# Optimization experiments

Measured on AMD Instinct MI355X. Metric: run time of the kernel, lower is better.

The kernel has to match this reference:

```python
import jax, jax.numpy as jnp
import numpy as np

B, NPER, F, D, E, NUM_STEPS = 256, 512, 256, 32, 524288, 4
N = B * NPER
INIT_TAU, TAU_SCALE, STEP_ALPHA = 0.1, 0.5, 5.0


def setup_inputs() -> dict:
    key = jax.random.key(0)
    ks = jax.random.split(key, 10)
    x_start = jax.random.uniform(ks[0], (N,), jnp.float32, 0.1, 1.0)   # strictly positive iterate
    x_solution = jax.random.uniform(ks[1], (N,), jnp.float32, 0.0, 1.0)
    q = jax.random.normal(ks[2], (N,), jnp.float32)
    edge_src = jax.random.randint(ks[3], (E,), 0, N, jnp.int32)
    edge_dst = jax.random.randint(ks[4], (E,), 0, N, jnp.int32)
    vals_batch = jnp.repeat(jnp.arange(B, dtype=jnp.int32), NPER)      # equal-sized graphs
    proj_matrix = jax.random.normal(ks[5], (B, NPER, F), jnp.float32) / np.float32(np.sqrt(NPER))
    W_in = jax.random.normal(ks[6], (2, D), jnp.float32) / np.float32(np.sqrt(2.0))
    b_in = jnp.zeros((D,), jnp.float32)
    W_msg = jax.random.normal(ks[7], (D, D), jnp.float32) / np.float32(np.sqrt(D))
    b_msg = jnp.zeros((D,), jnp.float32)
    W_out = jax.random.normal(ks[8], (D, 1), jnp.float32) / np.float32(np.sqrt(D))
    b_out = jnp.zeros((1,), jnp.float32)
    return {"x_start": x_start, "x_solution": x_solution, "q": q,
            "proj_matrix": proj_matrix, "W_in": W_in, "b_in": b_in,
            "W_msg": W_msg, "b_msg": b_msg, "W_out": W_out, "b_out": b_out,
            "edge_src": edge_src, "edge_dst": edge_dst, "vals_batch": vals_batch}


def _l1_normalize(x, batch):
    # per-graph L1 normalization: x / sum_i |x_i| over the graph segment
    s = jax.ops.segment_sum(jnp.abs(x), batch, num_segments=B)
    return x / (s[batch] + 1e-12)


def _line_search(x, d, batch, max_alpha):
    # largest per-graph alpha s.t. x + alpha*d >= 0, capped at max_alpha
    ratio = jnp.where(d < 0, x / jnp.maximum(-d, 1e-12), max_alpha)
    a = jnp.clip(jax.ops.segment_min(ratio, batch, num_segments=B), 0.0, max_alpha)
    return a[batch]  # gathered back to per-node


def _gnn(xs, q, edge_src, edge_dst, W_in, b_in, W_msg, b_msg, W_out, b_out):
    h = jax.nn.relu(jnp.stack([xs, q], axis=-1) @ W_in + b_in)      # [N, D]
    m = h[edge_src] @ W_msg + b_msg                                  # [E, D]
    agg = jax.ops.segment_sum(m, edge_dst, num_segments=N)          # [N, D]
    h2 = jax.nn.relu(h + agg)
    return h2 @ W_out[:, 0] + b_out[0]                               # [N]


def reference(x_start, x_solution, q, proj_matrix, W_in, b_in, W_msg, b_msg,
              W_out, b_out, edge_src, edge_dst, vals_batch):
    tau = INIT_TAU
    xs = x_start
    preds, labels = [], []
    for _ in range(NUM_STEPS):
        pred = _gnn(xs, q, edge_src, edge_dst, W_in, b_in, W_msg, b_msg, W_out, b_out)
        preds.append(pred)
        labels.append(_l1_normalize(x_solution - xs, vals_batch))
        p = _l1_normalize(jax.lax.stop_gradient(pred), vals_batch)   # .detach() in torch
        direction = p + 3.0 * tau / (xs + tau)
        tau = max(tau * TAU_SCALE, 1e-5)
        # to_dense_batch with equal graph sizes == reshape; project onto nullspace basis
        dd = direction.reshape(B, NPER)
        df = jnp.einsum('bnf,bn->bf', proj_matrix, dd)               # [B, F]
        pproj = jnp.einsum('bnf,bf->bn', proj_matrix, df).reshape(-1)  # [N]
        alpha = _line_search(xs, pproj, vals_batch, STEP_ALPHA) * 0.995
        xs = xs + alpha * pproj
    return jnp.stack(preds, axis=1), jnp.stack(labels, axis=1)       # each [N, NUM_STEPS]
```

## Files before the change

kernel.cpp:

```cpp
#include <hip/hip_runtime.h>

#define BB 256
#define NPER 512
#define FF 256
#define DD 32
#define EE 524288
#define NN (BB*NPER)
#define NSTEPS 4

__device__ __forceinline__ float bflo(unsigned u) { return __uint_as_float(u << 16); }
__device__ __forceinline__ float bfhi(unsigned u) { return __uint_as_float(u & 0xFFFF0000u); }
__device__ __forceinline__ unsigned rtn_bf16(unsigned u) {
    return (u + 0x7FFFu + ((u >> 16) & 1u)) >> 16;
}


__global__ void k_degpack(const int* __restrict__ dst, unsigned* __restrict__ deg,
                          const float* __restrict__ xs0, const float* __restrict__ q,
                          float2* __restrict__ xq) {
    int t = blockIdx.x * blockDim.x + threadIdx.x;
    if (t < NN) { float2 v; v.x = xs0[t]; v.y = q[t]; xq[t] = v; }
    atomicAdd(&deg[dst[t]], 1u);
}

__global__ __launch_bounds__(256) void k_alloc(const unsigned* __restrict__ deg,
                                               unsigned* __restrict__ gcur,
                                               unsigned* __restrict__ rowstart,
                                               unsigned* __restrict__ cursor) {
    __shared__ unsigned r[256];
    __shared__ unsigned base;
    int t = threadIdx.x;
    int i = blockIdx.x * 256 + t;
    unsigned d = deg[i];
    r[t] = d;
    __syncthreads();
    for (int o = 1; o < 256; o <<= 1) {
        unsigned v = (t >= o) ? r[t - o] : 0u;
        __syncthreads();
        r[t] += v;
        __syncthreads();
    }
    if (t == 255) base = atomicAdd(gcur, r[255]);
    __syncthreads();
    unsigned excl = r[t] - d + base;
    rowstart[i] = excl;
    cursor[i] = excl;
}

__global__ void k_fill(const int* __restrict__ src, const int* __restrict__ dst,
                       unsigned* __restrict__ cursor, int* __restrict__ csr_src) {
    int e = blockIdx.x * blockDim.x + threadIdx.x;
    unsigned pos = atomicAdd(&cursor[dst[e]], 1u);
    csr_src[pos] = src[e];
}

template<int MODE>
__global__ __launch_bounds__(1024) void k_mega(const float* __restrict__ Pf,
                                               unsigned short* __restrict__ Pbf,
                                               const float2* __restrict__ xq_cur,
                                               float2* __restrict__ xq_nxt,
                                               const float* __restrict__ xsol,
                                               const float* __restrict__ Win,
                                               const float* __restrict__ bin,
                                               const float* __restrict__ Wmsg,
                                               const float* __restrict__ bmsg,
                                               const float* __restrict__ Wout,
                                               const float* __restrict__ bout,
                                               const unsigned* __restrict__ rowstart,
                                               const unsigned* __restrict__ deg,
                                               const int* __restrict__ csr_src,
                                               float* __restrict__ out_preds,
                                               float* __restrict__ out_labels,
                                               float tau, int step) {
    __shared__ float pred_l[NPER];
    __shared__ float dd_l[NPER], x_l[NPER], pp_l[NPER];
    __shared__ float sl[16 * FF];
    __shared__ float dfl[FF];
    __shared__ float redA[16], redB[16];
    int b = blockIdx.x;
    int t = threadIdx.x;
    int w = t >> 6, lane = t & 63;
    int gbase = b * NPER;

    {
        int d = lane & 31;
        int half = lane >> 5;
        float w0 = Win[d], w1 = Win[DD + d], b0 = bin[d];
        float wcol[DD];
        #pragma unroll
        for (int k = 0; k < DD; ++k) wcol[k] = Wmsg[k * DD + d];
        float wo = Wout[d];
        for (int pass = 0; pass < 16; ++pass) {
            int node = pass * 32 + w * 2 + half;
            int i = gbase + node;
            unsigned rs = rowstart[i];
            unsigned dg = deg[i];
            unsigned nfull = dg < 32u ? dg : 32u;
            float xv = 0.f, qv = 0.f;
            if ((unsigned)d < nfull) {
                int sv = csr_src[rs + d];
                float2 v = xq_cur[sv];
                xv = v.x; qv = v.y;
            }
            float s = 0.f;
            for (unsigned j = 0; j < nfull; ++j) {
                float xj = __shfl(xv, (int)j, 32);
                float qj = __shfl(qv, (int)j, 32);
                s += fmaxf(xj * w0 + qj * w1 + b0, 0.f);
            }
            for (unsigned j = 32; j < dg; ++j) {
                int sv = csr_src[rs + j];
                float2 v = xq_cur[sv];
                s += fmaxf(v.x * w0 + v.y * w1 + b0, 0.f);
            }
            float2 self = xq_cur[i];
            float hval = fmaxf(self.x * w0 + self.y * w1 + b0, 0.f);
            float agg = (float)dg * bmsg[d];
            #pragma unroll
            for (int k = 0; k < DD; ++k) agg += __shfl(s, k, 32) * wcol[k];
            float h2 = fmaxf(hval + agg, 0.f);
            float v = h2 * wo;
            #pragma unroll
            for (int o = 16; o > 0; o >>= 1) v += __shfl_down(v, o, 32);
            if (d == 0) {
                float pr = v + bout[0];
                pred_l[node] = pr;
                out_preds[(size_t)i * NSTEPS + step] = pr;
            }
        }
    }
    __syncthreads();

    float x = 0.f, r = 0.f, p = 0.f, a1 = 0.f, a2 = 0.f;
    if (t < NPER) {
        x = xq_cur[gbase + t].x;
        r = xsol[gbase + t] - x;
        p = pred_l[t];
        a1 = fabsf(r); a2 = fabsf(p);
    }
    #pragma unroll
    for (int o = 32; o > 0; o >>= 1) {
        a1 += __shfl_down(a1, o, 64);
        a2 += __shfl_down(a2, o, 64);
    }
    if (lane == 0) { redA[w] = a1; redB[w] = a2; }
    __syncthreads();
    float Sr = 1e-12f, Sp = 1e-12f;
    #pragma unroll
    for (int k = 0; k < 16; ++k) { Sr += redA[k]; Sp += redB[k]; }
    if (t < NPER) out_labels[(size_t)(gbase + t) * NSTEPS + step] = r / Sr;
    if (MODE == 2) return;
    if (t < NPER) {
        x_l[t] = x;
        dd_l[t] = p / Sp + 3.0f * tau / (x + tau);
    }
    __syncthreads();

    size_t pbase = ((size_t)(gbase + w * 32)) * FF + 4 * lane;
    float4 acc = {0.f, 0.f, 0.f, 0.f};
    if (MODE == 0) {
        const float4* Pr = (const float4*)(Pf + pbase);
        uint2* Pw = (uint2*)(Pbf + pbase);
        #pragma unroll
        for (int nb = 0; nb < 4; ++nb) {
            float4 pv[8];
            #pragma unroll
            for (int k = 0; k < 8; ++k) pv[k] = Pr[(size_t)(nb * 8 + k) * 64];
            #pragma unroll
            for (int k = 0; k < 8; ++k) {
                int n = nb * 8 + k;
                float sc = dd_l[w * 32 + n];
                acc.x += pv[k].x * sc; acc.y += pv[k].y * sc;
                acc.z += pv[k].z * sc; acc.w += pv[k].w * sc;
                unsigned u0 = rtn_bf16(__float_as_uint(pv[k].x));
                unsigned u1 = rtn_bf16(__float_as_uint(pv[k].y));
                unsigned u2 = rtn_bf16(__float_as_uint(pv[k].z));
                unsigned u3 = rtn_bf16(__float_as_uint(pv[k].w));
                uint2 o2; o2.x = u0 | (u1 << 16); o2.y = u2 | (u3 << 16);
                Pw[(size_t)n * 64] = o2;
            }
        }
    } else {
        const uint2* Pr = (const uint2*)(Pbf + pbase);
        #pragma unroll
        for (int nb = 0; nb < 4; ++nb) {
            uint2 pv[8];
            #pragma unroll
            for (int k = 0; k < 8; ++k) pv[k] = Pr[(size_t)(nb * 8 + k) * 64];
            #pragma unroll
            for (int k = 0; k < 8; ++k) {
                float sc = dd_l[w * 32 + nb * 8 + k];
                acc.x += bflo(pv[k].x) * sc; acc.y += bfhi(pv[k].x) * sc;
                acc.z += bflo(pv[k].y) * sc; acc.w += bfhi(pv[k].y) * sc;
            }
        }
    }
    ((float4*)sl)[w * 64 + lane] = acc;
    __syncthreads();
    if (t < FF) {
        float v = 0.f;
        #pragma unroll
        for (int k = 0; k < 16; ++k) v += sl[k * FF + t];
        dfl[t] = v;
    }
    __syncthreads();

    {
        int g = t >> 5, l5 = t & 31;
        int w2 = g >> 1, h = g & 1;
        float4 dfa = ((const float4*)dfl)[l5 * 2];
        float4 dfb4 = ((const float4*)dfl)[l5 * 2 + 1];
        const uint4* Pbase = (const uint4*)(Pbf + (size_t)(gbase + w2 * 32) * FF) + l5;
        #pragma unroll
        for (int nb = 0; nb < 4; ++nb) {
            uint4 pv[4];
            int off[4];
            #pragma unroll
            for (int k = 0; k < 4; ++k) {
                int idx = nb * 4 + k;
                off[k] = (idx < 8) ? (16 + 8 * h + idx) : (8 * h + idx - 8);
                pv[k] = Pbase[(size_t)off[k] * 32];
            }
            #pragma unroll
            for (int k = 0; k < 4; ++k) {
                float a = bflo(pv[k].x) * dfa.x + bfhi(pv[k].x) * dfa.y
                        + bflo(pv[k].y) * dfa.z + bfhi(pv[k].y) * dfa.w
                        + bflo(pv[k].z) * dfb4.x + bfhi(pv[k].z) * dfb4.y
                        + bflo(pv[k].w) * dfb4.z + bfhi(pv[k].w) * dfb4.w;
                #pragma unroll
                for (int o = 16; o > 0; o >>= 1) a += __shfl_down(a, o, 32);
                if (l5 == 0) pp_l[w2 * 32 + off[k]] = a;
            }
        }
    }
    __syncthreads();

    float d = 0.f, m = 5.0f;
    if (t < NPER) {
        d = pp_l[t];
        m = (d < 0.f) ? (x_l[t] / fmaxf(-d, 1e-12f)) : 5.0f;
    }
    #pragma unroll
    for (int o = 32; o > 0; o >>= 1) m = fminf(m, __shfl_down(m, o, 64));
    if (lane == 0) redA[w] = m;
    __syncthreads();
    float mm = redA[0];
    #pragma unroll
    for (int k = 1; k < 16; ++k) mm = fminf(mm, redA[k]);
    float alpha = fminf(fmaxf(mm, 0.f), 5.0f) * 0.995f;
    if (t < NPER) {
        float2 o2;
        o2.x = x_l[t] + alpha * d;
        o2.y = xq_cur[gbase + t].y;
        xq_nxt[gbase + t] = o2;
    }
}


extern "C" void kernel_launch(void* const* d_in, const int* in_sizes, int n_in,
                              void* d_out, int out_size, void* d_ws, size_t ws_size,
                              hipStream_t stream) {
    const float* x_start = (const float*)d_in[0];
    const float* x_sol   = (const float*)d_in[1];
    const float* q       = (const float*)d_in[2];
    const float* P       = (const float*)d_in[3];
    const float* Win     = (const float*)d_in[4];
    const float* bin     = (const float*)d_in[5];
    const float* Wmsg    = (const float*)d_in[6];
    const float* bmsg    = (const float*)d_in[7];
    const float* Wout    = (const float*)d_in[8];
    const float* bout    = (const float*)d_in[9];
    const int*   esrc    = (const int*)d_in[10];
    const int*   edst    = (const int*)d_in[11];

    float* out_preds  = (float*)d_out;
    float* out_labels = (float*)d_out + (size_t)NN * NSTEPS;

    float* w = (float*)d_ws;
    unsigned* deg  = (unsigned*)w; w += NN;
    unsigned* gcur = (unsigned*)w; w += 2;
    float2* xqA = (float2*)w; w += 2 * (size_t)NN;
    float2* xqB = (float2*)w; w += 2 * (size_t)NN;
    unsigned* rowstart = (unsigned*)w; w += NN;
    unsigned* cursor   = (unsigned*)w; w += NN;
    int* csr_src       = (int*)w;      w += EE;
    unsigned short* Pbf = (unsigned short*)w;

    hipMemsetAsync(deg, 0, (NN + 2) * sizeof(unsigned), stream);
    k_degpack<<<EE / 256, 256, 0, stream>>>(edst, deg, x_start, q, xqA);
    k_alloc<<<NN / 256, 256, 0, stream>>>(deg, gcur, rowstart, cursor);
    k_fill<<<EE / 256, 256, 0, stream>>>(esrc, edst, cursor, csr_src);

    k_mega<0><<<BB, 1024, 0, stream>>>(P, Pbf, xqA, xqB, x_sol, Win, bin, Wmsg, bmsg,
                                       Wout, bout, rowstart, deg, csr_src,
                                       out_preds, out_labels, 0.1f, 0);
    k_mega<1><<<BB, 1024, 0, stream>>>(P, Pbf, xqB, xqA, x_sol, Win, bin, Wmsg, bmsg,
                                       Wout, bout, rowstart, deg, csr_src,
                                       out_preds, out_labels, 0.05f, 1);
    k_mega<1><<<BB, 1024, 0, stream>>>(P, Pbf, xqA, xqB, x_sol, Win, bin, Wmsg, bmsg,
                                       Wout, bout, rowstart, deg, csr_src,
                                       out_preds, out_labels, 0.025f, 2);
    k_mega<2><<<BB, 1024, 0, stream>>>(P, Pbf, xqB, (float2*)nullptr, x_sol, Win, bin,
                                       Wmsg, bmsg, Wout, bout, rowstart, deg, csr_src,
                                       out_preds, out_labels, 0.0125f, 3);
}
```

Before: 491.2 us.

## Cache half of bf16 projection slab in LDS and move final-step labels earlier

The first projection pass now also writes the bf16 projection rows for the first 256 nodes of each graph into a 128 KB shared-memory slab. The second projection pass reads those rows from LDS instead of re-reading them from global memory; the other half still comes from global. The last-step labels are now computed at the end of the third kernel from the updated iterate, so the final kernel only runs the GNN and returns early. The large LDS allocation may limit occupancy to one 1024-thread block per CU and adds extra shared-memory writes in the first pass.

```diff
diff --git a/kernel.cpp b/kernel.cpp
--- a/kernel.cpp
+++ b/kernel.cpp
@@ -71,12 +71,13 @@
                                                const int* __restrict__ csr_src,
                                                float* __restrict__ out_preds,
                                                float* __restrict__ out_labels,
-                                               float tau, int step) {
+                                               float tau, int step, int last) {
     __shared__ float pred_l[NPER];
     __shared__ float dd_l[NPER], x_l[NPER], pp_l[NPER];
     __shared__ float sl[16 * FF];
     __shared__ float dfl[FF];
     __shared__ float redA[16], redB[16];
+    __shared__ unsigned short slabL[(MODE < 2 ? 256 : 1) * FF];
     int b = blockIdx.x;
     int t = threadIdx.x;
     int w = t >> 6, lane = t & 63;
@@ -129,6 +130,7 @@
             }
         }
     }
+    if (MODE == 2) return;
     __syncthreads();
 
     float x = 0.f, r = 0.f, p = 0.f, a1 = 0.f, a2 = 0.f;
@@ -148,15 +150,15 @@
     float Sr = 1e-12f, Sp = 1e-12f;
     #pragma unroll
     for (int k = 0; k < 16; ++k) { Sr += redA[k]; Sp += redB[k]; }
-    if (t < NPER) out_labels[(size_t)(gbase + t) * NSTEPS + step] = r / Sr;
-    if (MODE == 2) return;
     if (t < NPER) {
+        out_labels[(size_t)(gbase + t) * NSTEPS + step] = r / Sr;
         x_l[t] = x;
         dd_l[t] = p / Sp + 3.0f * tau / (x + tau);
     }
     __syncthreads();
 
     size_t pbase = ((size_t)(gbase + w * 32)) * FF + 4 * lane;
+    unsigned short* slw = slabL + (size_t)(w * 32) * FF + 4 * lane;
     float4 acc = {0.f, 0.f, 0.f, 0.f};
     if (MODE == 0) {
         const float4* Pr = (const float4*)(Pf + pbase);
@@ -178,6 +180,7 @@
                 unsigned u3 = rtn_bf16(__float_as_uint(pv[k].w));
                 uint2 o2; o2.x = u0 | (u1 << 16); o2.y = u2 | (u3 << 16);
                 Pw[(size_t)n * 64] = o2;
+                if (w < 8) *(uint2*)(slw + (size_t)n * FF) = o2;
             }
         }
     } else {
@@ -189,9 +192,11 @@
             for (int k = 0; k < 8; ++k) pv[k] = Pr[(size_t)(nb * 8 + k) * 64];
             #pragma unroll
             for (int k = 0; k < 8; ++k) {
-                float sc = dd_l[w * 32 + nb * 8 + k];
+                int n = nb * 8 + k;
+                float sc = dd_l[w * 32 + n];
                 acc.x += bflo(pv[k].x) * sc; acc.y += bfhi(pv[k].x) * sc;
                 acc.z += bflo(pv[k].y) * sc; acc.w += bfhi(pv[k].y) * sc;
+                if (w < 8) *(uint2*)(slw + (size_t)n * FF) = pv[k];
             }
         }
     }
@@ -210,26 +215,51 @@
         int w2 = g >> 1, h = g & 1;
         float4 dfa = ((const float4*)dfl)[l5 * 2];
         float4 dfb4 = ((const float4*)dfl)[l5 * 2 + 1];
-        const uint4* Pbase = (const uint4*)(Pbf + (size_t)(gbase + w2 * 32) * FF) + l5;
-        #pragma unroll
-        for (int nb = 0; nb < 4; ++nb) {
-            uint4 pv[4];
-            int off[4];
-            #pragma unroll
-            for (int k = 0; k < 4; ++k) {
-                int idx = nb * 4 + k;
-                off[k] = (idx < 8) ? (16 + 8 * h + idx) : (8 * h + idx - 8);
-                pv[k] = Pbase[(size_t)off[k] * 32];
-            }
-            #pragma unroll
-            for (int k = 0; k < 4; ++k) {
-                float a = bflo(pv[k].x) * dfa.x + bfhi(pv[k].x) * dfa.y
-                        + bflo(pv[k].y) * dfa.z + bfhi(pv[k].y) * dfa.w
-                        + bflo(pv[k].z) * dfb4.x + bfhi(pv[k].z) * dfb4.y
-                        + bflo(pv[k].w) * dfb4.z + bfhi(pv[k].w) * dfb4.w;
+        if (g < 16) {
+            const uint4* Lb = (const uint4*)(slabL + (size_t)(w2 * 32) * FF) + l5;
+            #pragma unroll
+            for (int nb = 0; nb < 4; ++nb) {
+                uint4 pv[4];
+                int off[4];
                 #pragma unroll
-                for (int o = 16; o > 0; o >>= 1) a += __shfl_down(a, o, 32);
-                if (l5 == 0) pp_l[w2 * 32 + off[k]] = a;
+                for (int k = 0; k < 4; ++k) {
+                    int idx = nb * 4 + k;
+                    off[k] = (idx < 8) ? (16 + 8 * h + idx) : (8 * h + idx - 8);
+                    pv[k] = Lb[(size_t)off[k] * 32];
+                }
+                #pragma unroll
+                for (int k = 0; k < 4; ++k) {
+                    float a = bflo(pv[k].x) * dfa.x + bfhi(pv[k].x) * dfa.y
+                            + bflo(pv[k].y) * dfa.z + bfhi(pv[k].y) * dfa.w
+                            + bflo(pv[k].z) * dfb4.x + bfhi(pv[k].z) * dfb4.y
+                            + bflo(pv[k].w) * dfb4.z + bfhi(pv[k].w) * dfb4.w;
+                    #pragma unroll
+                    for (int o = 16; o > 0; o >>= 1) a += __shfl_down(a, o, 32);
+                    if (l5 == 0) pp_l[w2 * 32 + off[k]] = a;
+                }
+            }
+        } else {
+            const uint4* Pbase = (const uint4*)(Pbf + (size_t)(gbase + w2 * 32) * FF) + l5;
+            #pragma unroll
+            for (int nb = 0; nb < 4; ++nb) {
+                uint4 pv[4];
+                int off[4];
+                #pragma unroll
+                for (int k = 0; k < 4; ++k) {
+                    int idx = nb * 4 + k;
+                    off[k] = (idx < 8) ? (16 + 8 * h + idx) : (8 * h + idx - 8);
+                    pv[k] = Pbase[(size_t)off[k] * 32];
+                }
+                #pragma unroll
+                for (int k = 0; k < 4; ++k) {
+                    float a = bflo(pv[k].x) * dfa.x + bfhi(pv[k].x) * dfa.y
+                            + bflo(pv[k].y) * dfa.z + bfhi(pv[k].y) * dfa.w
+                            + bflo(pv[k].z) * dfb4.x + bfhi(pv[k].z) * dfb4.y
+                            + bflo(pv[k].w) * dfb4.z + bfhi(pv[k].w) * dfb4.w;
+                    #pragma unroll
+                    for (int o = 16; o > 0; o >>= 1) a += __shfl_down(a, o, 32);
+                    if (l5 == 0) pp_l[w2 * 32 + off[k]] = a;
+                }
             }
         }
     }
@@ -248,11 +278,26 @@
     #pragma unroll
     for (int k = 1; k < 16; ++k) mm = fminf(mm, redA[k]);
     float alpha = fminf(fmaxf(mm, 0.f), 5.0f) * 0.995f;
+    float xnew = 0.f;
     if (t < NPER) {
+        xnew = x_l[t] + alpha * d;
         float2 o2;
-        o2.x = x_l[t] + alpha * d;
+        o2.x = xnew;
         o2.y = xq_cur[gbase + t].y;
         xq_nxt[gbase + t] = o2;
+    }
+    if (last) {
+        float rr = 0.f, aa = 0.f;
+        if (t < NPER) { rr = xsol[gbase + t] - xnew; aa = fabsf(rr); }
+        #pragma unroll
+        for (int o = 32; o > 0; o >>= 1) aa += __shfl_down(aa, o, 64);
+        __syncthreads();
+        if (lane == 0) redB[w] = aa;
+        __syncthreads();
+        float Sr2 = 1e-12f;
+        #pragma unroll
+        for (int k = 0; k < 16; ++k) Sr2 += redB[k];
+        if (t < NPER) out_labels[(size_t)(gbase + t) * NSTEPS + (NSTEPS - 1)] = rr / Sr2;
     }
 }
 
@@ -293,14 +338,14 @@
 
     k_mega<0><<<BB, 1024, 0, stream>>>(P, Pbf, xqA, xqB, x_sol, Win, bin, Wmsg, bmsg,
                                        Wout, bout, rowstart, deg, csr_src,
-                                       out_preds, out_labels, 0.1f, 0);
+                                       out_preds, out_labels, 0.1f, 0, 0);
     k_mega<1><<<BB, 1024, 0, stream>>>(P, Pbf, xqB, xqA, x_sol, Win, bin, Wmsg, bmsg,
                                        Wout, bout, rowstart, deg, csr_src,
-                                       out_preds, out_labels, 0.05f, 1);
+                                       out_preds, out_labels, 0.05f, 1, 0);
     k_mega<1><<<BB, 1024, 0, stream>>>(P, Pbf, xqA, xqB, x_sol, Win, bin, Wmsg, bmsg,
                                        Wout, bout, rowstart, deg, csr_src,
-                                       out_preds, out_labels, 0.025f, 2);
+                                       out_preds, out_labels, 0.025f, 2, 1);
     k_mega<2><<<BB, 1024, 0, stream>>>(P, Pbf, xqB, (float2*)nullptr, x_sol, Win, bin,
                                        Wmsg, bmsg, Wout, bout, rowstart, deg, csr_src,
-                                       out_preds, out_labels, 0.0125f, 3);
-}
+                                       out_preds, out_labels, 0.0125f, 3, 0);
+}
```

Result: slower. 542.9 us (+10.5%).
